# Optimization experiments

Hardware: AMD Instinct MI355X
Metric: run time of the kernel (lower is better)

Reference implementation:

```python
import jax, jax.numpy as jnp
import numpy as np

B, S, H = 128, 512, 1024
SEP = 2


def setup_inputs() -> dict:
    key = jax.random.key(0)
    k1, k2, k3, k4 = jax.random.split(key, 4)
    hidden_states = jax.random.normal(k1, (B, S, H), dtype=jnp.float32)
    # per-sample segment boundaries: <s> title </s></s> lead </s> pad...
    title_end = jax.random.randint(k2, (B,), 5, 200)          # pos of first </s>
    lead_end = jax.random.randint(k3, (B,), 250, S - 2)        # pos of third </s>
    tokens = jax.random.randint(k4, (B, S), 5, 64000)          # avoid SEP=2 collisions
    rows = jnp.arange(B)
    input_ids = tokens.at[:, 0].set(0)                          # <s>
    input_ids = input_ids.at[rows, title_end].set(SEP)
    input_ids = input_ids.at[rows, title_end + 1].set(SEP)
    input_ids = input_ids.at[rows, lead_end].set(SEP)
    attention_mask = (jnp.arange(S)[None, :] <= lead_end[:, None]).astype(jnp.int32)
    return {
        "hidden_states": hidden_states,
        "input_ids": input_ids.astype(jnp.int64),
        "attention_mask": attention_mask,
        "sep_token_id": SEP,
    }


def reference(hidden_states, input_ids, attention_mask, sep_token_id):
    # hidden_states: (B,S,H); input_ids, attention_mask: (B,S)
    b, s, h = hidden_states.shape
    sep = input_ids == sep_token_id                      # (B,S) bool
    cnt = jnp.cumsum(sep.astype(jnp.int32), axis=1)      # inclusive sep count
    num_seps = cnt[:, -1]                                # (B,)

    def pos_of(k):
        # index of k-th separator (argmax of first True); 0 if absent
        return jnp.argmax(sep & (cnt == k), axis=1)

    p1, p2, p3 = pos_of(1), pos_of(2), pos_of(3)
    mask_len = attention_mask.sum(axis=1)
    lead_end = jnp.where(num_seps >= 3, p3, mask_len)    # (B,)
    lead_start = p2 + 1

    idx = jnp.arange(s)[None, :]                         # (1,S)
    valid = (num_seps >= 2)[:, None]
    title_mask = (idx >= 1) & (idx < p1[:, None]) & valid
    lead_mask = (idx >= lead_start[:, None]) & (idx < lead_end[:, None]) & valid

    cls = hidden_states[:, 0, :]                         # fallback: <s> token

    def masked_mean(m):
        mf = m.astype(hidden_states.dtype)               # (B,S)
        ssum = jnp.einsum('bs,bsh->bh', mf, hidden_states)
        c = mf.sum(axis=1, keepdims=True)                # (B,1)
        return jnp.where(c > 0, ssum / jnp.maximum(c, 1.0), cls)

    return masked_mean(title_mask), masked_mean(lead_mask)
```

## Files before the change

kernel.cpp:

```cpp
#include <hip/hip_runtime.h>

#define BB 128
#define SS 512
#define HH 1024
#define NB 16

typedef float f32x4 __attribute__((ext_vector_type(4)));


__device__ __forceinline__ int4 compute_meta(const int* __restrict__ ids,
                                             const int* __restrict__ attn,
                                             int b, int sep) {
    __shared__ unsigned long long words[SS / 64];
    __shared__ int sh_p[4];
    __shared__ int sh_mask;
    const int t = threadIdx.x;
    const int* row = ids + b * SS;
    const int tok0 = row[t];
    const int tok1 = row[t + 256];
    const unsigned long long b0 = __ballot(tok0 == sep);
    const unsigned long long b1 = __ballot(tok1 == sep);
    if ((t & 63) == 0) {
        words[t >> 6] = b0;
        words[4 + (t >> 6)] = b1;
    }
    if (t == 0) sh_mask = 0;
    __syncthreads();
    if (t == 0) {
        int cnt = 0, p1 = 0, p2 = 0, p3 = 0;
        for (int i = 0; i < SS / 64; ++i) {
            unsigned long long word = words[i];
            while (word && cnt < 3) {
                const int pos = i * 64 + __builtin_ctzll(word);
                ++cnt;
                if (cnt == 1) p1 = pos;
                else if (cnt == 2) p2 = pos;
                else p3 = pos;
                word &= word - 1;
            }
        }
        sh_p[0] = p1; sh_p[1] = p2; sh_p[2] = p3; sh_p[3] = cnt;
    }
    __syncthreads();
    const int cnt = sh_p[3];
    if (cnt < 3) {
        const int* arow = attn + b * SS;
        atomicAdd(&sh_mask, arow[t] + arow[t + 256]);
        __syncthreads();
    }
    int4 m;
    if (cnt >= 2) {
        m.x = 1;
        m.y = max(sh_p[0], 1);
        m.z = sh_p[1] + 1;
        const int e = (cnt >= 3) ? sh_p[2] : sh_mask;
        m.w = max(e, m.z);
    } else {
        m.x = 0; m.y = 0; m.z = 0; m.w = 0;
    }
    return m;
}

__global__ void __launch_bounds__(256)
seg_sum_balanced(const float* __restrict__ hs,
                 const int* __restrict__ ids,
                 const int* __restrict__ attn,
                 const int* __restrict__ sep_tok,
                 int4* __restrict__ meta,
                 float* __restrict__ partials) {
    const int nb = blockIdx.x;
    const int b  = blockIdx.y;
    const int4 m = compute_meta(ids, attn, b, sep_tok[0]);
    const int t_len = m.y - m.x;
    const int l_len = m.w - m.z;
    const int T = t_len + l_len;

    if (nb == 0 && threadIdx.x == 0) meta[b] = m;

    const int u0 = (nb * T) / NB;
    const int u1 = ((nb + 1) * T) / NB;

    const int h4 = threadIdx.x;
    const f32x4* base = (const f32x4*)(hs + (size_t)b * SS * HH);
    f32x4* p = (f32x4*)(partials + (size_t)(b * NB + nb) * 2 * HH);

    const int tA = u0, tB = min(u1, t_len);
    if (tA < tB) {
        f32x4 a = {0.f, 0.f, 0.f, 0.f};
        #pragma unroll 4
        for (int u = tA; u < tB; ++u)
            a += base[(size_t)(m.x + u) * (HH / 4) + h4];
        p[h4] = a;
    }
    const int lA = max(u0, t_len), lB = u1;
    if (lA < lB) {
        f32x4 a = {0.f, 0.f, 0.f, 0.f};
        #pragma unroll 4
        for (int u = lA; u < lB; ++u)
            a += base[(size_t)(m.z + (u - t_len)) * (HH / 4) + h4];
        p[HH / 4 + h4] = a;
    }
}

__global__ void __launch_bounds__(512)
seg_final_lite(const float* __restrict__ hs,
               const int4* __restrict__ meta,
               const float* __restrict__ partials,
               float* __restrict__ out) {
    const int b    = blockIdx.x;
    const int span = threadIdx.x >> 8;
    const int h4   = threadIdx.x & 255;

    const int4 m = meta[b];
    const int t_len = m.y - m.x;
    const int l_len = m.w - m.z;
    const int T = t_len + l_len;
    const int cntr = (span == 0) ? t_len : l_len;

    f32x4 a = {0.f, 0.f, 0.f, 0.f};
    #pragma unroll
    for (int k = 0; k < NB; ++k) {
        const int v0 = (k * T) / NB;
        const int v1 = ((k + 1) * T) / NB;
        bool valid;
        if (span == 0) valid = v0 < min(v1, t_len);
        else           valid = max(v0, t_len) < v1;
        if (valid) {
            const f32x4* p = (const f32x4*)(partials +
                (size_t)(b * NB + k) * 2 * HH + (size_t)span * HH);
            a += p[h4];
        }
    }

    f32x4 o;
    if (cntr > 0) {
        o = a / (float)cntr;
    } else {
        o = ((const f32x4*)(hs + (size_t)b * SS * HH))[h4];
    }
    ((f32x4*)out)[(size_t)(span * BB + b) * (HH / 4) + h4] = o;
}

extern "C" void kernel_launch(void* const* d_in, const int* in_sizes, int n_in,
                              void* d_out, int out_size, void* d_ws, size_t ws_size,
                              hipStream_t stream) {
    const float* hs  = (const float*)d_in[0];
    const int*   ids = (const int*)d_in[1];
    const int*   am  = (const int*)d_in[2];
    const int*   sep = (const int*)d_in[3];
    float* out = (float*)d_out;

    int4*  meta     = (int4*)d_ws;
    float* partials = (float*)((char*)d_ws + 4096);

    seg_sum_balanced<<<dim3(NB, BB), 256, 0, stream>>>(hs, ids, am, sep,
                                                       meta, partials);
    seg_final_lite<<<BB, 512, 0, stream>>>(hs, meta, partials, out);
}
```

Measured before the change: 44.60 us.

## Split separator metadata computation into a dedicated kernel before segment sum

Moves the per-row separator scan and attention-mask count out of the segment-sum kernel into a separate seg_meta kernel with one 512-thread block per row. Previously each of the 16 blocks per row recomputed the metadata, with several block barriers before any hidden-state loads could start. The sum kernel now just reads the precomputed meta. The cost is an extra kernel launch and a serialization point between the stages. The attention mask is now always counted, not only when fewer than three separators are found.

Measured after the change: 47.78 us. 1.07x slower.

```diff
diff --git a/kernel.cpp b/kernel.cpp
--- a/kernel.cpp
+++ b/kernel.cpp
@@ -8,25 +8,29 @@
 typedef float f32x4 __attribute__((ext_vector_type(4)));
 
 
-__device__ __forceinline__ int4 compute_meta(const int* __restrict__ ids,
-                                             const int* __restrict__ attn,
-                                             int b, int sep) {
+__global__ void __launch_bounds__(512)
+seg_meta(const int* __restrict__ ids,
+         const int* __restrict__ attn,
+         const int* __restrict__ sep_tok,
+         int4* __restrict__ meta) {
     __shared__ unsigned long long words[SS / 64];
-    __shared__ int sh_p[4];
     __shared__ int sh_mask;
-    const int t = threadIdx.x;
-    const int* row = ids + b * SS;
-    const int tok0 = row[t];
-    const int tok1 = row[t + 256];
-    const unsigned long long b0 = __ballot(tok0 == sep);
-    const unsigned long long b1 = __ballot(tok1 == sep);
-    if ((t & 63) == 0) {
-        words[t >> 6] = b0;
-        words[4 + (t >> 6)] = b1;
-    }
-    if (t == 0) sh_mask = 0;
+    const int b = blockIdx.x;
+    const int s = threadIdx.x;
+
+    if (s == 0) sh_mask = 0;
     __syncthreads();
-    if (t == 0) {
+
+    const int sep = sep_tok[0];
+    const int tok = ids[b * SS + s];
+    const int am  = attn[b * SS + s];
+
+    const unsigned long long bal = __ballot(tok == sep);
+    if ((s & 63) == 0) words[s >> 6] = bal;
+    if (am) atomicAdd(&sh_mask, 1);
+    __syncthreads();
+
+    if (s == 0) {
         int cnt = 0, p1 = 0, p2 = 0, p3 = 0;
         for (int i = 0; i < SS / 64; ++i) {
             unsigned long long word = words[i];
@@ -39,43 +43,30 @@
                 word &= word - 1;
             }
         }
-        sh_p[0] = p1; sh_p[1] = p2; sh_p[2] = p3; sh_p[3] = cnt;
+        int4 m;
+        if (cnt >= 2) {
+            m.x = 1;
+            m.y = max(p1, 1);
+            m.z = p2 + 1;
+            const int e = (cnt >= 3) ? p3 : sh_mask;
+            m.w = max(e, m.z);
+        } else {
+            m.x = 0; m.y = 0; m.z = 0; m.w = 0;
+        }
+        meta[b] = m;
     }
-    __syncthreads();
-    const int cnt = sh_p[3];
-    if (cnt < 3) {
-        const int* arow = attn + b * SS;
-        atomicAdd(&sh_mask, arow[t] + arow[t + 256]);
-        __syncthreads();
-    }
-    int4 m;
-    if (cnt >= 2) {
-        m.x = 1;
-        m.y = max(sh_p[0], 1);
-        m.z = sh_p[1] + 1;
-        const int e = (cnt >= 3) ? sh_p[2] : sh_mask;
-        m.w = max(e, m.z);
-    } else {
-        m.x = 0; m.y = 0; m.z = 0; m.w = 0;
-    }
-    return m;
 }
 
 __global__ void __launch_bounds__(256)
 seg_sum_balanced(const float* __restrict__ hs,
-                 const int* __restrict__ ids,
-                 const int* __restrict__ attn,
-                 const int* __restrict__ sep_tok,
-                 int4* __restrict__ meta,
+                 const int4* __restrict__ meta,
                  float* __restrict__ partials) {
     const int nb = blockIdx.x;
     const int b  = blockIdx.y;
-    const int4 m = compute_meta(ids, attn, b, sep_tok[0]);
+    const int4 m = meta[b];
     const int t_len = m.y - m.x;
     const int l_len = m.w - m.z;
     const int T = t_len + l_len;
-
-    if (nb == 0 && threadIdx.x == 0) meta[b] = m;
 
     const int u0 = (nb * T) / NB;
     const int u1 = ((nb + 1) * T) / NB;
@@ -153,7 +144,7 @@
     int4*  meta     = (int4*)d_ws;
     float* partials = (float*)((char*)d_ws + 4096);
 
-    seg_sum_balanced<<<dim3(NB, BB), 256, 0, stream>>>(hs, ids, am, sep,
-                                                       meta, partials);
+    seg_meta<<<BB, SS, 0, stream>>>(ids, am, sep, meta);
+    seg_sum_balanced<<<dim3(NB, BB), 256, 0, stream>>>(hs, meta, partials);
     seg_final_lite<<<BB, 512, 0, stream>>>(hs, meta, partials, out);
 }
```
